# Kernel optimization log

Hardware: AMD Instinct MI355X
Metric: run time of the kernel (lower is better)

The kernel has to match this reference:

```python
import jax, jax.numpy as jnp
from jax import lax
import numpy as np

T = 100  # number of binarization thresholds, as in nn.Module (linspace(0,1,100))
THRESHOLDS = jnp.linspace(0.0, 1.0, T)


def _count_components(binimg):
    """4-connected component count per image via iterative min-label propagation.
    binimg: [N,H,W] float in {0,1}. Returns [N] int32 component counts.
    Equivalent math to the source's recursive DFS flood fill, vectorized."""
    N, H, W = binimg.shape
    fg = binimg > 0
    BIG = H * W  # sentinel label for background
    idx = jnp.arange(H * W, dtype=jnp.int32).reshape(H, W)
    lab0 = jnp.where(fg, idx[None], jnp.int32(BIG))

    def prop(lab):
        p = jnp.pad(lab, ((0, 0), (1, 1), (1, 1)), constant_values=BIG)
        nmin = jnp.minimum(jnp.minimum(p[:, :-2, 1:-1], p[:, 2:, 1:-1]),
                           jnp.minimum(p[:, 1:-1, :-2], p[:, 1:-1, 2:]))
        return jnp.where(fg, jnp.minimum(lab, nmin), jnp.int32(BIG))

    def cond(c):
        return ~c[1]

    def body(c):
        lab = c[0]
        new = prop(prop(prop(lab)))  # 3 propagation steps per convergence check
        return (new, jnp.all(new == lab))

    lab, _ = lax.while_loop(cond, body, (lab0, jnp.array(False)))
    # each component keeps exactly one pixel whose label equals its own index
    return jnp.sum(fg & (lab == idx[None]), axis=(1, 2)).astype(jnp.int32)


def _betti(prob):
    """prob: [R,H,W] -> [T,R,2] (b0, b1) per threshold per region.
    b1 = b0 - euler, euler = #pixels - #4-neighbor edges (as in source)."""
    R, H, W = prob.shape
    binz = (prob[None] > THRESHOLDS[:, None, None, None]).astype(jnp.float32)  # [T,R,H,W]
    flat = binz.reshape(T * R, H, W)
    b0 = lax.stop_gradient(_count_components(flat)).astype(jnp.float32).reshape(T, R)
    pix = flat.sum((1, 2))
    edges = (flat[:, :-1] * flat[:, 1:]).sum((1, 2)) + (flat[:, :, :-1] * flat[:, :, 1:]).sum((1, 2))
    euler = (pix - edges).reshape(T, R)
    b1 = b0 - euler
    return jnp.stack([b0, b1], axis=-1)  # [T,R,2]


def setup_inputs() -> dict:
    key = jax.random.key(0)
    k1, k2 = jax.random.split(key)
    three_class_prob = jax.random.uniform(k1, (4, 3, 128, 128), dtype=jnp.float32)
    selected_regions = jnp.arange(4, dtype=jnp.int64)
    gt_barcodes = jax.random.uniform(k2, (4, 6, T - 1, 2), dtype=jnp.float32)
    return {"three_class_prob": three_class_prob,
            "selected_regions": selected_regions,
            "gt_barcodes": gt_barcodes}


def reference(three_class_prob, selected_regions, gt_barcodes):
    sel = three_class_prob[selected_regions]  # [R,3,H,W]
    inside = _betti(sel[:, 0])     # channel 0
    boundary = _betti(sel[:, 1])   # channel 1
    union = inside                 # source uses channel 0:1 again -> same values
    codes = jnp.concatenate([inside, boundary, union], axis=-1)  # [T,R,6]
    # barcode extraction: birth at increases of the betti curve, death at decreases
    d = codes[1:] - codes[:-1]                 # [T-1,R,6]
    th = THRESHOLDS[:-1, None, None]
    birth = jnp.where(d > 0, th, 0.0)
    death = jnp.where(d < 0, th, 0.0)
    barcodes = jnp.stack([birth, death], axis=-1).transpose(1, 2, 0, 3)  # [R,6,T-1,2]
    # fixed-shape matching: pair barcodes sorted by birth time (Hungarian surrogate)
    ord_b = jnp.argsort(barcodes[..., 0], axis=-1)
    ord_g = jnp.argsort(gt_barcodes[..., 0], axis=-1)
    bs = jnp.take_along_axis(barcodes, ord_b[..., None], axis=-2)
    gs = jnp.take_along_axis(gt_barcodes, ord_g[..., None], axis=-2)
    matched_diff = jnp.sum(jnp.abs(bs - gs), axis=-1)                  # [R,6,T-1]
    unmatched_len = jnp.sum(barcodes[..., 1] - barcodes[..., 0], axis=-1)  # [R,6]
    return jnp.mean(matched_diff) + jnp.mean(unmatched_len)
```

## Files before the change

### kernel.cpp

```cpp
#include <hip/hip_runtime.h>

typedef unsigned long long u64;

#define FLAG_M1 0x13579BDFu
#define FLAG_M2 0x2468ACE1u

__device__ __forceinline__ int find_root(int* L, int a){
    int p = L[a];
    while(p != a){
        int gp = L[p];
        if(gp != p) L[a] = gp;
        a = p; p = gp;
    }
    return a;
}

__device__ __forceinline__ int unite(int* L, int a, int b){
    while(true){
        a = find_root(L, a);
        b = find_root(L, b);
        if(a == b) return 0;
        int hi = (a > b) ? a : b;
        int lo = (a > b) ? b : a;
        int old = atomicCAS(&L[hi], hi, lo);
        if(old == hi) return 1;
        a = old; b = lo;
    }
}

__device__ __forceinline__ void ccl_body(const float* __restrict__ prob,
                                         const int*   __restrict__ sel,
                                         float*       __restrict__ betti,
                                         unsigned*    __restrict__ flags,
                                         float*       __restrict__ out,
                                         u64* M, u64* S, int* Pr, int* L, int* red,
                                         int tid, int bid){
    if(bid == 0 && tid == 0) atomicExch(out, 0.0f);
    const int ch = bid / 400, t = (bid % 400) >> 2, r = bid & 3;
    const float th = (float)t / 99.0f;
    const float* img = prob + (size_t)(sel[r] * 3 + ch) * 16384;

    const int w = tid;
    {
        const float4* imgv = (const float4*)img;
        u64 mw = 0ULL;
        #pragma unroll
        for(int k = 0; k < 16; k++){
            const float4 v = imgv[w * 16 + k];
            const unsigned nib = (unsigned)(v.x > th)
                               | ((unsigned)(v.y > th) << 1)
                               | ((unsigned)(v.z > th) << 2)
                               | ((unsigned)(v.w > th) << 3);
            mw |= (u64)nib << (4 * k);
        }
        M[w] = mw;
    }
    __syncthreads();

    const int lane = tid & 63, wave = tid >> 6;
    const int row = w >> 1, half = w & 1;
    const u64 m = M[w];
    const u64 lcar = half ? (M[w - 1] >> 63) : 0ULL;
    const u64 s = m & ~((m << 1) | lcar);
    S[w] = s;
    int pix   = __popcll(m);
    int edges = __popcll(m & ((m << 1) | lcar));
    const u64 va = (row > 0) ? M[w - 2] : 0ULL;
    edges += __popcll(m & va);
    const int runs = __popcll(s);
    u64 csm = 0ULL;
    if(row > 0){
        const u64 c = m & va;
        const u64 ccar = half ? ((M[w - 1] & M[w - 3]) >> 63) : 0ULL;
        csm = c & ~((c << 1) | ccar);
    }

    int incl = runs;
    for(int off = 1; off < 64; off <<= 1){
        int n = __shfl_up(incl, off, 64);
        if(lane >= off) incl += n;
    }
    if(lane == 63) red[wave] = incl;
    __syncthreads();
    int woff = 0;
    for(int k = 0; k < wave; k++) woff += red[k];
    const int excl = woff + incl - runs;
    Pr[w] = excl;
    if(w == 255) Pr[256] = excl + runs;
    const u64 sa = (row > 0) ? S[w - 2] : 0ULL;
    __syncthreads();
    const int R = Pr[256];
    const int Pa = (row > 0) ? Pr[w - 2] : 0;

    {
        int4* L4 = (int4*)L;
        const int n4 = (R + 3) >> 2;
        for(int i = tid; i < n4; i += 256){ int b = i * 4; L4[i] = make_int4(b, b+1, b+2, b+3); }
    }
    __syncthreads();

    int merges = 0;
    {
        u64 cs = csm;
        while(cs){
            const int x = __ffsll(cs) - 1;
            cs &= cs - 1;
            const u64 lm = (2ULL << x) - 1;
            const int nb = excl + __popcll(s  & lm) - 1;
            const int na = Pa   + __popcll(sa & lm) - 1;
            merges += unite(L, na, nb);
        }
    }

    int v0 = pix, v1 = edges, v2 = merges;
    for(int off = 32; off; off >>= 1){
        v0 += __shfl_down(v0, off, 64);
        v1 += __shfl_down(v1, off, 64);
        v2 += __shfl_down(v2, off, 64);
    }
    __syncthreads();
    if(lane == 0){ red[wave*3] = v0; red[wave*3+1] = v1; red[wave*3+2] = v2; }
    __syncthreads();
    if(tid == 0){
        int P = 0, E = 0, MG = 0;
        for(int k = 0; k < 4; k++){ P += red[k*3]; E += red[k*3+1]; MG += red[k*3+2]; }
        const float b0f = (float)(R - MG);
        const float b1f = b0f - ((float)P - (float)E);
        const size_t o = (((size_t)ch * 100 + t) * 4 + r) * 2;
        __hip_atomic_store(&betti[o],     b0f, __ATOMIC_RELAXED, __HIP_MEMORY_SCOPE_AGENT);
        __hip_atomic_store(&betti[o + 1], b1f, __ATOMIC_RELAXED, __HIP_MEMORY_SCOPE_AGENT);
        unsigned* f = flags + (size_t)bid * 8;
        __hip_atomic_store(&f[0], FLAG_M1, __ATOMIC_RELEASE, __HIP_MEMORY_SCOPE_AGENT);
        __hip_atomic_store(&f[4], FLAG_M2, __ATOMIC_RELEASE, __HIP_MEMORY_SCOPE_AGENT);
    }
}

__device__ __forceinline__ void rows_body(const float* __restrict__ betti,
                                          const float* __restrict__ gt,
                                          float*       __restrict__ out,
                                          int row, int tid, float* fsh){
    float* codes = fsh;
    float* birth = fsh + 100;
    float* bs0   = fsh + 199;
    float* bs1   = fsh + 298;
    float* gs0   = fsh + 397;
    float* gs1   = fsh + 496;
    float* gsh   = fsh + 595;
    float* redf  = fsh + 793;
    const int r = row / 6, j = row % 6;
    const int chmap[6] = {0, 0, 1, 1, 0, 0};
    const int ch = chmap[j], comp = j & 1;

    if(tid < 100)
        codes[tid] = __hip_atomic_load(&betti[(((size_t)ch * 100 + tid) * 4 + r) * 2 + comp],
                                       __ATOMIC_RELAXED, __HIP_MEMORY_SCOPE_AGENT);
    const float* g = gt + (size_t)row * 198;
    for(int i = tid; i < 198; i += 256) gsh[i] = g[i];
    __syncthreads();

    float b = 0.f, d = 0.f;
    if(tid < 99){
        const float dv = codes[tid + 1] - codes[tid];
        const float thv = (float)tid / 99.0f;
        b = (dv > 0.f) ? thv : 0.f;
        d = (dv < 0.f) ? thv : 0.f;
        birth[tid] = b;
    }
    __syncthreads();

    if(tid < 99){
        int zb = 0, tz = 0;
        for(int k = 0; k < 99; k++){
            const int z = (birth[k] == 0.f) ? 1 : 0;
            tz += z;
            if(k < tid) zb += z;
        }
        const int pos = (b == 0.f) ? zb : (tz + tid - zb);
        bs0[pos] = b; bs1[pos] = d;

        const float gb = gsh[tid * 2];
        int rank = 0;
        for(int k = 0; k < 99; k++){
            const float o = gsh[k * 2];
            rank += (o < gb || (o == gb && k < tid)) ? 1 : 0;
        }
        gs0[rank] = gb; gs1[rank] = gsh[tid * 2 + 1];
    }
    __syncthreads();

    float mm = 0.f, u = 0.f;
    if(tid < 99){
        mm = fabsf(bs0[tid] - gs0[tid]) + fabsf(bs1[tid] - gs1[tid]);
        u = d - b;
    }
    for(int off = 32; off; off >>= 1){
        mm += __shfl_down(mm, off, 64);
        u  += __shfl_down(u,  off, 64);
    }
    if((tid & 63) == 0){ redf[(tid >> 6) * 2] = mm; redf[(tid >> 6) * 2 + 1] = u; }
    __syncthreads();
    if(tid == 0)
        atomicAdd(out, (redf[0] + redf[2] + redf[4] + redf[6]) / 2376.0f
                     + (redf[1] + redf[3] + redf[5] + redf[7]) / 24.0f);
}

__global__ __launch_bounds__(256) void fused_kernel(const float* __restrict__ prob,
                                                    const int*   __restrict__ sel,
                                                    const float* __restrict__ gt,
                                                    float*       __restrict__ betti,
                                                    unsigned*    __restrict__ flags,
                                                    float*       __restrict__ out){
    __shared__ u64 M[256];
    __shared__ u64 S[256];
    __shared__ int Pr[257];
    __shared__ int L[6400];
    __shared__ int red[12];
    const int tid = threadIdx.x, bid = blockIdx.x;

    if(bid < 800){
        ccl_body(prob, sel, betti, flags, out, M, S, Pr, L, red, tid, bid);
        return;
    }

    const int row = bid - 800;
    const int r = row / 6, j = row % 6;
    const int chmap[6] = {0, 0, 1, 1, 0, 0};
    const int ch = chmap[j];

    if(tid <= 100){
        const int pb = (tid < 100) ? (ch * 400 + tid * 4 + r) : 0;
        unsigned* f = flags + (size_t)pb * 8;
        while(__hip_atomic_load(&f[0], __ATOMIC_ACQUIRE, __HIP_MEMORY_SCOPE_AGENT) != FLAG_M1 ||
              __hip_atomic_load(&f[4], __ATOMIC_ACQUIRE, __HIP_MEMORY_SCOPE_AGENT) != FLAG_M2){
            __builtin_amdgcn_s_sleep(8);
        }
    }
    __syncthreads();

    rows_body(betti, gt, out, row, tid, (float*)L);
}

extern "C" void kernel_launch(void* const* d_in, const int* in_sizes, int n_in,
                              void* d_out, int out_size, void* d_ws, size_t ws_size,
                              hipStream_t stream){
    const float* prob = (const float*)d_in[0];
    const int*   sel  = (const int*)d_in[1];
    const float* gt   = (const float*)d_in[2];
    float*    betti = (float*)d_ws;
    unsigned* flags = (unsigned*)((char*)d_ws + 8192);

    fused_kernel<<<824, 256, 0, stream>>>(prob, sel, gt, betti, flags, (float*)d_out);
}
```

Measured before the change: 94.04 us.

## Coalesce image loads via shared atomicOr bitmask and interleave union-find root walks

The image threshold load now has consecutive threads read consecutive float4s, so global loads are coalesced. Each thread's nibble is merged into a shared 32-bit bitmask word with atomicOr, which needs a zero-init pass and an extra barrier. The union-find root search now walks both roots in one interleaved loop with path splitting, to overlap the dependent LDS loads of the two chains. The cost is shared-memory atomic contention, since 8 threads write into the same word.

```diff
diff --git a/kernel.cpp b/kernel.cpp
--- a/kernel.cpp
+++ b/kernel.cpp
@@ -5,24 +5,21 @@
 #define FLAG_M1 0x13579BDFu
 #define FLAG_M2 0x2468ACE1u
 
-__device__ __forceinline__ int find_root(int* L, int a){
-    int p = L[a];
-    while(p != a){
-        int gp = L[p];
-        if(gp != p) L[a] = gp;
-        a = p; p = gp;
-    }
-    return a;
-}
-
 __device__ __forceinline__ int unite(int* L, int a, int b){
     while(true){
-        a = find_root(L, a);
-        b = find_root(L, b);
+        int pva = -1, pvb = -1;
+        while(true){
+            const int pa = L[a];
+            const int pb = L[b];
+            const bool ma = (pa != a), mb = (pb != b);
+            if(!ma && !mb) break;
+            if(ma){ if(pva >= 0) L[pva] = pa; pva = a; a = pa; }
+            if(mb){ if(pvb >= 0) L[pvb] = pb; pvb = b; b = pb; }
+        }
         if(a == b) return 0;
-        int hi = (a > b) ? a : b;
-        int lo = (a > b) ? b : a;
-        int old = atomicCAS(&L[hi], hi, lo);
+        const int hi = (a > b) ? a : b;
+        const int lo = (a > b) ? b : a;
+        const int old = atomicCAS(&L[hi], hi, lo);
         if(old == hi) return 1;
         a = old; b = lo;
     }
@@ -40,24 +37,28 @@
     const float th = (float)t / 99.0f;
     const float* img = prob + (size_t)(sel[r] * 3 + ch) * 16384;
 
-    const int w = tid;
+    unsigned* M32 = (unsigned*)M;
+    M32[tid] = 0u; M32[tid + 256] = 0u;
+    __syncthreads();
+
     {
         const float4* imgv = (const float4*)img;
-        u64 mw = 0ULL;
+        const unsigned u0 = tid >> 3;
+        const unsigned sh = 4u * (tid & 7);
         #pragma unroll
         for(int k = 0; k < 16; k++){
-            const float4 v = imgv[w * 16 + k];
+            const float4 v = imgv[tid + 256 * k];
             const unsigned nib = (unsigned)(v.x > th)
                                | ((unsigned)(v.y > th) << 1)
                                | ((unsigned)(v.z > th) << 2)
                                | ((unsigned)(v.w > th) << 3);
-            mw |= (u64)nib << (4 * k);
-        }
-        M[w] = mw;
+            if(nib) atomicOr(&M32[u0 + 32 * k], nib << sh);
+        }
     }
     __syncthreads();
 
     const int lane = tid & 63, wave = tid >> 6;
+    const int w = tid;
     const int row = w >> 1, half = w & 1;
     const u64 m = M[w];
     const u64 lcar = half ? (M[w - 1] >> 63) : 0ULL;
```

After: 101.6 us. 8.1% more time.

## Compact vertical merge pairs into shared worklist for balanced union across threads

Applied to the files above, without the earlier changes.

Each thread's run-overlap merge pairs are counted with a second prefix sum packed into the upper 16 bits of the existing run scan, then written into a shared-memory worklist. All 256 threads then process the worklist round-robin, so union work is spread evenly instead of depending on how many merge segments each row-half holds. An overflow path falls back to the per-thread loop when the list exceeds its capacity. The cost is about 20KB of extra LDS per block, which may reduce occupancy, plus the packing and extra stores.

```diff
diff --git a/kernel.cpp b/kernel.cpp
--- a/kernel.cpp
+++ b/kernel.cpp
@@ -4,6 +4,7 @@
 
 #define FLAG_M1 0x13579BDFu
 #define FLAG_M2 0x2468ACE1u
+#define WL_CAP  4928
 
 __device__ __forceinline__ int find_root(int* L, int a){
     int p = L[a];
@@ -33,7 +34,8 @@
                                          float*       __restrict__ betti,
                                          unsigned*    __restrict__ flags,
                                          float*       __restrict__ out,
-                                         u64* M, u64* S, int* Pr, int* L, int* red,
+                                         u64* M, u64* S, int* Pr, int* L,
+                                         unsigned* WL, int* red,
                                          int tid, int bid){
     if(bid == 0 && tid == 0) atomicExch(out, 0.0f);
     const int ch = bid / 400, t = (bid % 400) >> 2, r = bid & 3;
@@ -74,8 +76,10 @@
         const u64 ccar = half ? ((M[w - 1] & M[w - 3]) >> 63) : 0ULL;
         csm = c & ~((c << 1) | ccar);
     }
-
-    int incl = runs;
+    const int nseg = __popcll(csm);
+
+    const int packed = runs | (nseg << 16);
+    int incl = packed;
     for(int off = 1; off < 64; off <<= 1){
         int n = __shfl_up(incl, off, 64);
         if(lane >= off) incl += n;
@@ -84,31 +88,57 @@
     __syncthreads();
     int woff = 0;
     for(int k = 0; k < wave; k++) woff += red[k];
-    const int excl = woff + incl - runs;
-    Pr[w] = excl;
-    if(w == 255) Pr[256] = excl + runs;
+    const int exclP = woff + incl - packed;
+    Pr[w] = exclP;
+    if(w == 255) Pr[256] = exclP + packed;
     const u64 sa = (row > 0) ? S[w - 2] : 0ULL;
     __syncthreads();
-    const int R = Pr[256];
-    const int Pa = (row > 0) ? Pr[w - 2] : 0;
+    const int RK = Pr[256];
+    const int R  = RK & 0xFFFF;
+    const int K  = (int)((unsigned)RK >> 16);
+    const int excl  = exclP & 0xFFFF;
+    const int sexcl = (int)((unsigned)exclP >> 16);
+    const int Pa = (row > 0) ? (Pr[w - 2] & 0xFFFF) : 0;
 
     {
         int4* L4 = (int4*)L;
         const int n4 = (R + 3) >> 2;
         for(int i = tid; i < n4; i += 256){ int b = i * 4; L4[i] = make_int4(b, b+1, b+2, b+3); }
     }
-    __syncthreads();
-
-    int merges = 0;
-    {
+    {
+        int slot = sexcl;
         u64 cs = csm;
-        while(cs){
+        while(cs && slot < WL_CAP){
             const int x = __ffsll(cs) - 1;
             cs &= cs - 1;
             const u64 lm = (2ULL << x) - 1;
             const int nb = excl + __popcll(s  & lm) - 1;
             const int na = Pa   + __popcll(sa & lm) - 1;
-            merges += unite(L, na, nb);
+            WL[slot++] = ((unsigned)na << 13) | (unsigned)nb;
+        }
+    }
+    __syncthreads();
+
+    int merges = 0;
+    {
+        const int KC = (K < WL_CAP) ? K : WL_CAP;
+        for(int i = tid; i < KC; i += 256){
+            const unsigned e = WL[i];
+            merges += unite(L, (int)(e >> 13), (int)(e & 0x1FFFu));
+        }
+        if(K > WL_CAP){
+            u64 cs = csm; int idx = sexcl;
+            while(cs){
+                const int x = __ffsll(cs) - 1;
+                cs &= cs - 1;
+                if(idx >= WL_CAP){
+                    const u64 lm = (2ULL << x) - 1;
+                    const int nb = excl + __popcll(s  & lm) - 1;
+                    const int na = Pa   + __popcll(sa & lm) - 1;
+                    merges += unite(L, na, nb);
+                }
+                idx++;
+            }
         }
     }
 
@@ -214,11 +244,12 @@
     __shared__ u64 S[256];
     __shared__ int Pr[257];
     __shared__ int L[6400];
+    __shared__ unsigned WL[WL_CAP];
     __shared__ int red[12];
     const int tid = threadIdx.x, bid = blockIdx.x;
 
     if(bid < 800){
-        ccl_body(prob, sel, betti, flags, out, M, S, Pr, L, red, tid, bid);
+        ccl_body(prob, sel, betti, flags, out, M, S, Pr, L, WL, red, tid, bid);
         return;
     }
 
```

Result: no change. 93.83 us (-0.2%).
